# Kernel tuning notes

Measured on AMD Instinct MI355X. Metric: run time of the kernel, lower is better.

## Reference

```python
import jax, jax.numpy as jnp
import jax.scipy.ndimage
import numpy as np

RES = 256       # image / detector resolution (must be even)
N_ANGLES = 256  # number of projection angles
BATCH = 8


def setup_inputs() -> dict:
    key = jax.random.key(0)
    imgs = jax.random.normal(key, (BATCH, RES, RES), dtype=jnp.float32)
    # torch-radon typically uses angles uniformly spanning [0, pi)
    angles = jnp.asarray(np.linspace(0.0, np.pi, N_ANGLES, endpoint=False), dtype=jnp.float32)
    return {"imgs": imgs, "angles": angles}


def _radon(imgs, angles):
    """Parallel-beam Radon transform via bilinear (texture-style) ray sampling.

    imgs:   [B, RES, RES]
    angles: [A]
    returns sinogram [B, A, RES]
    """
    res = imgs.shape[-1]
    c = (res - 1) / 2.0  # image center in pixel-index space
    s = jnp.arange(res, dtype=jnp.float32) - c  # detector offsets (ray lateral position)
    t = jnp.arange(res, dtype=jnp.float32) - c  # unit-step samples along each ray
    cos = jnp.cos(angles)  # [A]
    sin = jnp.sin(angles)
    # Rotated ray sample point (x, y) = R(theta) @ (s, t), centered coords, shape [A, S, T]
    x = s[None, :, None] * cos[:, None, None] - t[None, None, :] * sin[:, None, None]
    y = s[None, :, None] * sin[:, None, None] + t[None, None, :] * cos[:, None, None]
    coords = jnp.stack([y + c, x + c])  # [2, A, S, T] -> (row, col) index space

    def sample(img):
        # bilinear sampling, zero outside the image (matches border-zero texture fetch)
        return jax.scipy.ndimage.map_coordinates(img, coords, order=1, mode='constant', cval=0.0)

    vals = jax.vmap(sample)(imgs)  # [B, A, S, T]
    return vals.sum(axis=-1)       # unit step length -> ray integral, sinogram [B, A, S]


def reference(imgs, angles):
    return _radon(imgs, angles)
```

## Files before the change

kernel.cpp:

```cpp
#include <hip/hip_runtime.h>
#include <hip/hip_fp16.h>
#include <math.h>

#define RES 256
#define TPAD 364
#define N_ANGLES 256
#define NA2 129
#define BATCH 8
#define ROWB (TPAD * 16)

typedef _Float16 h2 __attribute__((ext_vector_type(2)));
__device__ inline h2 u2h(unsigned u) { return __builtin_bit_cast(h2, u); }

__global__ void prep_pack(const float* __restrict__ imgs,
                          unsigned int* __restrict__ W) {
    int idx = blockIdx.x * blockDim.x + threadIdx.x;
    const int total = 4 * TPAD * TPAD * 4;
    if (idx >= total) return;
    int pair  = idx & 3;
    int px    = (idx >> 2) % (TPAD * TPAD);
    int plane = (idx >> 2) / (TPAD * TPAD);
    int orient = plane >> 1, side = plane & 1;
    int ct = px % TPAD, rt = px / TPAD;
    int ri = rt - 53, ci = ct - 53;
    int row, col;
    if (orient == 0) { row = ri; col = side ? (255 - ci) : ci; }
    else             { row = ci; col = side ? (255 - ri) : ri; }
    float v0 = 0.0f, v1 = 0.0f;
    if ((unsigned)row < RES && (unsigned)col < RES) {
        const float* p = imgs + ((size_t)(pair * 2) * RES + row) * RES + col;
        v0 = p[0];
        v1 = p[RES * RES];
    }
    __half2 h = __halves2half2(__float2half_rn(v0), __float2half_rn(v1));
    W[((size_t)plane * TPAD * TPAD + px) * 4 + pair] =
        *reinterpret_cast<unsigned int*>(&h);
}

__global__ __launch_bounds__(128) void radon_kernel(
        const char* __restrict__ TEX,
        const float* __restrict__ angles,
        __half* __restrict__ part) {
    const int tid  = threadIdx.x;
    const int tap  = tid & 3;
    const int tpar = (tid >> 2) & 1;
    const int s    = blockIdx.y * 16 + (tid >> 3);
    const int a    = blockIdx.x;
    const int z    = blockIdx.z;

    float theta = angles[a];
    float sn, cs;
    sincosf(theta, &sn, &cs);

    const size_t planeB = (size_t)TPAD * TPAD * 16;
    float Rs, Rt, Cs, Ct;
    const char* bN;
    const char* bF;
    if (fabsf(cs) >= fabsf(sn)) {
        Rs = sn; Rt = cs;  Cs = cs; Ct = -sn;
        bN = TEX;              bF = TEX + planeB;
    } else {
        Rs = cs; Rt = -sn; Cs = sn; Ct = cs;
        bN = TEX + 2 * planeB; bF = TEX + 3 * planeB;
    }

    const float s_c = (float)s - 127.5f;
    const float pr0 = fmaf(s_c, Rs, 180.5f) - 127.5f * Rt;
    const float pc0 = fmaf(s_c, Cs, 180.5f) - 127.5f * Ct;

    const float LO = 52.0f, HI = 309.0f;
    float tmin = 0.0f, tmax = 255.0f;
    {
        float inv = 1.0f / Rt;
        float ta = (LO - pr0) * inv, tb = (HI - pr0) * inv;
        tmin = fmaxf(tmin, fminf(ta, tb));
        tmax = fminf(tmax, fmaxf(ta, tb));
    }
    if (fabsf(Ct) > 1e-6f) {
        float inv = 1.0f / Ct;
        float ta = (LO - pc0) * inv, tb = (HI - pc0) * inv;
        tmin = fmaxf(tmin, fminf(ta, tb));
        tmax = fminf(tmax, fmaxf(ta, tb));
    } else if (!(pc0 >= LO && pc0 <= HI)) {
        tmax = -1.0f;
    }

    const float tb0 = (float)(z * 128 + tpar);
    int i0 = (int)ceilf((tmin - tb0) * 0.5f);
    int i1 = (int)floorf((tmax - tb0) * 0.5f);
    i0 = max(i0, 0);
    i1 = min(i1, 63);
    int c0 = i0 >> 4, c1 = i1 >> 4;
    if (i1 < i0) { c0 = 1; c1 = 0; }

    const int dr = tap >> 1, dc = tap & 1;
    const unsigned tapoff = (unsigned)(dr * ROWB + dc * 16);
    const float xb = dc ? 0.0f : 1.0f, xs = dc ? 1.0f : -1.0f;
    const float yb = dr ? 0.0f : 1.0f, ys = dr ? 1.0f : -1.0f;

    float a0=0.f,a1=0.f,a2=0.f,a3=0.f,a4=0.f,a5=0.f,a6=0.f,a7=0.f;
    float b0=0.f,b1=0.f,b2=0.f,b3=0.f,b4=0.f,b5=0.f,b6=0.f,b7=0.f;

    for (int c = c0; c <= c1; ++c) {
        h2 n0={},n1={},n2={},n3={}, f0={},f1={},f2={},f3={};
        float tf = fmaf(32.0f, (float)c, tb0);
        #pragma unroll
        for (int k = 0; k < 16; ++k) {
            float ppr = fmaf(tf, Rt, pr0);
            float ppc = fmaf(tf, Ct, pc0);
            tf += 2.0f;
            float wy, wx;
            int ir, ic;
            asm("v_fract_f32 %0, %1"       : "=v"(wy) : "v"(ppr));
            asm("v_fract_f32 %0, %1"       : "=v"(wx) : "v"(ppc));
            asm("v_cvt_flr_i32_f32 %0, %1" : "=v"(ir) : "v"(ppr));
            asm("v_cvt_flr_i32_f32 %0, %1" : "=v"(ic) : "v"(ppc));
            unsigned x = ((unsigned)ic << 4) + tapoff;
            unsigned bo;
            asm("v_mad_u32_u24 %0, %1, %2, %3"
                : "=v"(bo) : "v"(ir), "s"(ROWB), "v"(x));
            float w = fmaf(xs, wx, xb) * fmaf(ys, wy, yb);
            auto pkr = __builtin_amdgcn_cvt_pkrtz(w, w);
            h2 wv = __builtin_bit_cast(h2, pkr);
            uint4 qn = *(const uint4*)(bN + bo);
            uint4 qf = *(const uint4*)(bF + bo);
            n0 = wv * u2h(qn.x) + n0;
            n1 = wv * u2h(qn.y) + n1;
            n2 = wv * u2h(qn.z) + n2;
            n3 = wv * u2h(qn.w) + n3;
            f0 = wv * u2h(qf.x) + f0;
            f1 = wv * u2h(qf.y) + f1;
            f2 = wv * u2h(qf.z) + f2;
            f3 = wv * u2h(qf.w) + f3;
        }
        a0 += (float)n0.x; a1 += (float)n0.y; a2 += (float)n1.x; a3 += (float)n1.y;
        a4 += (float)n2.x; a5 += (float)n2.y; a6 += (float)n3.x; a7 += (float)n3.y;
        b0 += (float)f0.x; b1 += (float)f0.y; b2 += (float)f1.x; b3 += (float)f1.y;
        b4 += (float)f2.x; b5 += (float)f2.y; b6 += (float)f3.x; b7 += (float)f3.y;
    }

    #define RED(x) { x += __shfl_xor(x, 1); x += __shfl_xor(x, 2); x += __shfl_xor(x, 4); }
    RED(a0) RED(a1) RED(a2) RED(a3) RED(a4) RED(a5) RED(a6) RED(a7)
    RED(b0) RED(b1) RED(b2) RED(b3) RED(b4) RED(b5) RED(b6) RED(b7)
    #undef RED

    if ((tid & 7) == 0) {
        const size_t AR = (size_t)N_ANGLES * RES;
        const size_t zb = (size_t)z * BATCH * AR;
        size_t pbase = zb + (size_t)a * RES + s;
        part[pbase         ] = __float2half(a0);
        part[pbase + 1 * AR] = __float2half(a1);
        part[pbase + 2 * AR] = __float2half(a2);
        part[pbase + 3 * AR] = __float2half(a3);
        part[pbase + 4 * AR] = __float2half(a4);
        part[pbase + 5 * AR] = __float2half(a5);
        part[pbase + 6 * AR] = __float2half(a6);
        part[pbase + 7 * AR] = __float2half(a7);
        if (a != 0) {
            size_t qbase = zb + (size_t)(N_ANGLES - a) * RES + s;
            part[qbase         ] = __float2half(b0);
            part[qbase + 1 * AR] = __float2half(b1);
            part[qbase + 2 * AR] = __float2half(b2);
            part[qbase + 3 * AR] = __float2half(b3);
            part[qbase + 4 * AR] = __float2half(b4);
            part[qbase + 5 * AR] = __float2half(b5);
            part[qbase + 6 * AR] = __float2half(b6);
            part[qbase + 7 * AR] = __float2half(b7);
        }
    }
}

__global__ void combine(const __half2* __restrict__ p, float2* __restrict__ out) {
    const int n2 = BATCH * N_ANGLES * RES / 2;
    int i = blockIdx.x * blockDim.x + threadIdx.x;
    if (i < n2) {
        float2 x = __half22float2(p[i]);
        float2 y = __half22float2(p[i + n2]);
        out[i] = make_float2(x.x + y.x, x.y + y.y);
    }
}

extern "C" void kernel_launch(void* const* d_in, const int* in_sizes, int n_in,
                              void* d_out, int out_size, void* d_ws, size_t ws_size,
                              hipStream_t stream) {
    const float* imgs   = (const float*)d_in[0];
    const float* angles = (const float*)d_in[1];
    float* out = (float*)d_out;

    const size_t planeB = (size_t)TPAD * TPAD * 16;
    char*   TEX  = (char*)d_ws;
    __half* part = (__half*)(TEX + 4 * planeB);

    const int prep_total = 4 * TPAD * TPAD * 4;
    prep_pack<<<(prep_total + 255) / 256, 256, 0, stream>>>(
        imgs, (unsigned int*)TEX);

    dim3 grid(NA2, 16, 2);
    radon_kernel<<<grid, 128, 0, stream>>>(TEX, angles, part);

    const int n2 = BATCH * N_ANGLES * RES / 2;
    combine<<<(n2 + 255) / 256, 256, 0, stream>>>((const __half2*)part, (float2*)out);
}
```

Measured before the change: 62.25 us.

## Stage sheared image band in LDS and gather bilinear taps from shared memory

The radon kernel now cooperatively loads, per block, a sheared band of the packed texture (72 rows by 32 columns, both planes) into LDS with an XOR swizzle. Each thread then does all four bilinear taps from shared memory, where before four lanes each fetched one tap from global memory. The ray is split into 4 t-chunks of 64 with 256 threads per block, and partial sums are reduced through shuffles and an LDS scratch. The combine kernel now sums four partials instead of two. This trades global gather traffic for LDS reuse, at the cost of a staging pass, extra syncs, half-precision accumulation across chunks and more partial-buffer traffic.

```diff
diff --git a/kernel.cpp b/kernel.cpp
--- a/kernel.cpp
+++ b/kernel.cpp
@@ -9,8 +9,16 @@
 #define BATCH 8
 #define ROWB (TPAD * 16)
 
+#define SCH 16
+#define TCH 64
+#define NTC 4
+#define BROWS 72
+#define PLANE_TEX (BROWS * 32)
+#define PLANE_B (PLANE_TEX * 16)
+
 typedef _Float16 h2 __attribute__((ext_vector_type(2)));
 __device__ inline h2 u2h(unsigned u) { return __builtin_bit_cast(h2, u); }
+__device__ inline unsigned h2u(h2 h) { return __builtin_bit_cast(unsigned, h); }
 
 __global__ void prep_pack(const float* __restrict__ imgs,
                           unsigned int* __restrict__ W) {
@@ -37,36 +45,49 @@
         *reinterpret_cast<unsigned int*>(&h);
 }
 
-__global__ __launch_bounds__(128) void radon_kernel(
+__global__ __launch_bounds__(256) void radon_kernel(
         const char* __restrict__ TEX,
         const float* __restrict__ angles,
         __half* __restrict__ part) {
-    const int tid  = threadIdx.x;
-    const int tap  = tid & 3;
-    const int tpar = (tid >> 2) & 1;
-    const int s    = blockIdx.y * 16 + (tid >> 3);
-    const int a    = blockIdx.x;
-    const int z    = blockIdx.z;
+    __shared__ uint4 band[2 * PLANE_TEX];
+
+    const int tid = threadIdx.x;
+    const int sl  = tid & 15;
+    const int tl  = tid >> 4;
+    const int a   = blockIdx.x;
+    const int s0  = blockIdx.y * SCH;
+    const int tc  = blockIdx.z;
+    const int t0  = tc * TCH;
 
     float theta = angles[a];
     float sn, cs;
     sincosf(theta, &sn, &cs);
 
-    const size_t planeB = (size_t)TPAD * TPAD * 16;
+    const size_t planeGB = (size_t)TPAD * TPAD * 16;
     float Rs, Rt, Cs, Ct;
-    const char* bN;
-    const char* bF;
+    const char *gN, *gF;
     if (fabsf(cs) >= fabsf(sn)) {
         Rs = sn; Rt = cs;  Cs = cs; Ct = -sn;
-        bN = TEX;              bF = TEX + planeB;
+        gN = TEX;                gF = TEX + planeGB;
     } else {
         Rs = cs; Rt = -sn; Cs = sn; Ct = cs;
-        bN = TEX + 2 * planeB; bF = TEX + 3 * planeB;
-    }
-
-    const float s_c = (float)s - 127.5f;
-    const float pr0 = fmaf(s_c, Rs, 180.5f) - 127.5f * Rt;
-    const float pc0 = fmaf(s_c, Cs, 180.5f) - 127.5f * Ct;
+        gN = TEX + 2 * planeGB;  gF = TEX + 3 * planeGB;
+    }
+
+    const float m = Ct / Rt;
+    const float smc = (float)s0 - 120.0f;
+    const float tmc = (float)t0 - 96.0f;
+    const float prc = fmaf(smc, Rs, fmaf(tmc, Rt, 180.5f));
+    const float pcc = fmaf(smc, Cs, fmaf(tmc, Ct, 180.5f));
+    const int   r0  = (int)floorf(prc - 7.5f * fabsf(Rs) - 31.5f * fabsf(Rt)) - 2;
+    const float ku  = Cs - m * Rs;
+    const float ubase = (pcc - m * prc) - 7.5f * fabsf(ku) - 3.0f;
+
+    const float s_c = (float)(s0 + sl) - 127.5f;
+    const float prA = fmaf(s_c, Rs, 180.5f);
+    const float pcA = fmaf(s_c, Cs, 180.5f);
+    const float pr0 = prA - 127.5f * Rt;
+    const float pc0 = pcA - 127.5f * Ct;
 
     const float LO = 52.0f, HI = 309.0f;
     float tmin = 0.0f, tmax = 255.0f;
@@ -84,89 +105,130 @@
     } else if (!(pc0 >= LO && pc0 <= HI)) {
         tmax = -1.0f;
     }
-
-    const float tb0 = (float)(z * 128 + tpar);
-    int i0 = (int)ceilf((tmin - tb0) * 0.5f);
-    int i1 = (int)floorf((tmax - tb0) * 0.5f);
-    i0 = max(i0, 0);
-    i1 = min(i1, 63);
-    int c0 = i0 >> 4, c1 = i1 >> 4;
-    if (i1 < i0) { c0 = 1; c1 = 0; }
-
-    const int dr = tap >> 1, dc = tap & 1;
-    const unsigned tapoff = (unsigned)(dr * ROWB + dc * 16);
-    const float xb = dc ? 0.0f : 1.0f, xs = dc ? 1.0f : -1.0f;
-    const float yb = dr ? 0.0f : 1.0f, ys = dr ? 1.0f : -1.0f;
-
-    float a0=0.f,a1=0.f,a2=0.f,a3=0.f,a4=0.f,a5=0.f,a6=0.f,a7=0.f;
-    float b0=0.f,b1=0.f,b2=0.f,b3=0.f,b4=0.f,b5=0.f,b6=0.f,b7=0.f;
-
-    for (int c = c0; c <= c1; ++c) {
-        h2 n0={},n1={},n2={},n3={}, f0={},f1={},f2={},f3={};
-        float tf = fmaf(32.0f, (float)c, tb0);
+    int ik0 = (int)ceilf((tmin - (float)(t0 + tl)) * 0.0625f);
+    int ik1 = (int)floorf((tmax - (float)(t0 + tl)) * 0.0625f);
+    int kmin = max(ik0, 0), kmax = min(ik1, 3);
+
+    h2 nA0 = {}, nA1 = {}, nA2 = {}, nA3 = {};
+    h2 fA0 = {}, fA1 = {}, fA2 = {}, fA3 = {};
+
+    int anywork = __syncthreads_or(kmin <= kmax);
+    if (anywork) {
         #pragma unroll
-        for (int k = 0; k < 16; ++k) {
-            float ppr = fmaf(tf, Rt, pr0);
-            float ppc = fmaf(tf, Ct, pc0);
-            tf += 2.0f;
+        for (int it = 0; it < 9; ++it) {
+            int idx = tid + it * 256;
+            int rs = idx >> 5, j = idx & 31;
+            int r  = r0 + rs;
+            int cb = (int)floorf(fmaf((float)r, m, ubase));
+            int c  = cb + j;
+            uint4 vn = make_uint4(0u, 0u, 0u, 0u);
+            uint4 vf = vn;
+            if (r >= 53 && r <= 308 && c >= 53 && c <= 308) {
+                size_t go = (size_t)r * ROWB + (size_t)c * 16;
+                vn = *(const uint4*)(gN + go);
+                vf = *(const uint4*)(gF + go);
+            }
+            unsigned ad = ((unsigned)rs << 9)
+                        + ((((unsigned)c & 31u) << 4) ^ ((((unsigned)(rs * 3)) & 31u) << 4));
+            *(uint4*)((char*)band + ad) = vn;
+            *(uint4*)((char*)band + ad + PLANE_B) = vf;
+        }
+        __syncthreads();
+
+        const char* bb = (const char*)band;
+        float tcur = (float)(t0 + tl + 16 * kmin) - 127.5f;
+        for (int k = kmin; k <= kmax; ++k) {
+            float ppr = fmaf(tcur, Rt, prA);
+            float ppc = fmaf(tcur, Ct, pcA);
+            tcur += 16.0f;
             float wy, wx;
             int ir, ic;
             asm("v_fract_f32 %0, %1"       : "=v"(wy) : "v"(ppr));
             asm("v_fract_f32 %0, %1"       : "=v"(wx) : "v"(ppc));
             asm("v_cvt_flr_i32_f32 %0, %1" : "=v"(ir) : "v"(ppr));
             asm("v_cvt_flr_i32_f32 %0, %1" : "=v"(ic) : "v"(ppc));
-            unsigned x = ((unsigned)ic << 4) + tapoff;
-            unsigned bo;
-            asm("v_mad_u32_u24 %0, %1, %2, %3"
-                : "=v"(bo) : "v"(ir), "s"(ROWB), "v"(x));
-            float w = fmaf(xs, wx, xb) * fmaf(ys, wy, yb);
-            auto pkr = __builtin_amdgcn_cvt_pkrtz(w, w);
-            h2 wv = __builtin_bit_cast(h2, pkr);
-            uint4 qn = *(const uint4*)(bN + bo);
-            uint4 qf = *(const uint4*)(bF + bo);
-            n0 = wv * u2h(qn.x) + n0;
-            n1 = wv * u2h(qn.y) + n1;
-            n2 = wv * u2h(qn.z) + n2;
-            n3 = wv * u2h(qn.w) + n3;
-            f0 = wv * u2h(qf.x) + f0;
-            f1 = wv * u2h(qf.y) + f1;
-            f2 = wv * u2h(qf.z) + f2;
-            f3 = wv * u2h(qf.w) + f3;
+            int rs0 = ir - r0;
+            unsigned row0 = (unsigned)rs0 << 9;
+            unsigned row1 = row0 + 512u;
+            unsigned sw0 = (((unsigned)(rs0 * 3)) & 31u) << 4;
+            unsigned sw1 = (((unsigned)(rs0 * 3 + 3)) & 31u) << 4;
+            unsigned u0 = ((unsigned)ic & 31u) << 4;
+            unsigned u1 = ((unsigned)(ic + 1) & 31u) << 4;
+            unsigned a00 = row0 + (u0 ^ sw0), a01 = row0 + (u1 ^ sw0);
+            unsigned a10 = row1 + (u0 ^ sw1), a11 = row1 + (u1 ^ sw1);
+
+            uint4 n00 = *(const uint4*)(bb + a00);
+            uint4 n01 = *(const uint4*)(bb + a01);
+            uint4 n10 = *(const uint4*)(bb + a10);
+            uint4 n11 = *(const uint4*)(bb + a11);
+            uint4 f00 = *(const uint4*)(bb + a00 + PLANE_B);
+            uint4 f01 = *(const uint4*)(bb + a01 + PLANE_B);
+            uint4 f10 = *(const uint4*)(bb + a10 + PLANE_B);
+            uint4 f11 = *(const uint4*)(bb + a11 + PLANE_B);
+
+            float wx1 = 1.0f - wx, wy1 = 1.0f - wy;
+            float w00f = wy1 * wx1, w01f = wy1 * wx;
+            float w10f = wy  * wx1, w11f = wy  * wx;
+            auto pk = [](float x) {
+                auto v = __builtin_amdgcn_cvt_pkrtz(x, x);
+                return __builtin_bit_cast(h2, v);
+            };
+            h2 w00 = pk(w00f), w01 = pk(w01f), w10 = pk(w10f), w11 = pk(w11f);
+
+            nA0 = w00 * u2h(n00.x) + nA0;  nA1 = w00 * u2h(n00.y) + nA1;
+            nA2 = w00 * u2h(n00.z) + nA2;  nA3 = w00 * u2h(n00.w) + nA3;
+            nA0 = w01 * u2h(n01.x) + nA0;  nA1 = w01 * u2h(n01.y) + nA1;
+            nA2 = w01 * u2h(n01.z) + nA2;  nA3 = w01 * u2h(n01.w) + nA3;
+            nA0 = w10 * u2h(n10.x) + nA0;  nA1 = w10 * u2h(n10.y) + nA1;
+            nA2 = w10 * u2h(n10.z) + nA2;  nA3 = w10 * u2h(n10.w) + nA3;
+            nA0 = w11 * u2h(n11.x) + nA0;  nA1 = w11 * u2h(n11.y) + nA1;
+            nA2 = w11 * u2h(n11.z) + nA2;  nA3 = w11 * u2h(n11.w) + nA3;
+
+            fA0 = w00 * u2h(f00.x) + fA0;  fA1 = w00 * u2h(f00.y) + fA1;
+            fA2 = w00 * u2h(f00.z) + fA2;  fA3 = w00 * u2h(f00.w) + fA3;
+            fA0 = w01 * u2h(f01.x) + fA0;  fA1 = w01 * u2h(f01.y) + fA1;
+            fA2 = w01 * u2h(f01.z) + fA2;  fA3 = w01 * u2h(f01.w) + fA3;
+            fA0 = w10 * u2h(f10.x) + fA0;  fA1 = w10 * u2h(f10.y) + fA1;
+            fA2 = w10 * u2h(f10.z) + fA2;  fA3 = w10 * u2h(f10.w) + fA3;
+            fA0 = w11 * u2h(f11.x) + fA0;  fA1 = w11 * u2h(f11.y) + fA1;
+            fA2 = w11 * u2h(f11.z) + fA2;  fA3 = w11 * u2h(f11.w) + fA3;
         }
-        a0 += (float)n0.x; a1 += (float)n0.y; a2 += (float)n1.x; a3 += (float)n1.y;
-        a4 += (float)n2.x; a5 += (float)n2.y; a6 += (float)n3.x; a7 += (float)n3.y;
-        b0 += (float)f0.x; b1 += (float)f0.y; b2 += (float)f1.x; b3 += (float)f1.y;
-        b4 += (float)f2.x; b5 += (float)f2.y; b6 += (float)f3.x; b7 += (float)f3.y;
-    }
-
-    #define RED(x) { x += __shfl_xor(x, 1); x += __shfl_xor(x, 2); x += __shfl_xor(x, 4); }
-    RED(a0) RED(a1) RED(a2) RED(a3) RED(a4) RED(a5) RED(a6) RED(a7)
-    RED(b0) RED(b1) RED(b2) RED(b3) RED(b4) RED(b5) RED(b6) RED(b7)
-    #undef RED
-
-    if ((tid & 7) == 0) {
-        const size_t AR = (size_t)N_ANGLES * RES;
-        const size_t zb = (size_t)z * BATCH * AR;
-        size_t pbase = zb + (size_t)a * RES + s;
-        part[pbase         ] = __float2half(a0);
-        part[pbase + 1 * AR] = __float2half(a1);
-        part[pbase + 2 * AR] = __float2half(a2);
-        part[pbase + 3 * AR] = __float2half(a3);
-        part[pbase + 4 * AR] = __float2half(a4);
-        part[pbase + 5 * AR] = __float2half(a5);
-        part[pbase + 6 * AR] = __float2half(a6);
-        part[pbase + 7 * AR] = __float2half(a7);
-        if (a != 0) {
-            size_t qbase = zb + (size_t)(N_ANGLES - a) * RES + s;
-            part[qbase         ] = __float2half(b0);
-            part[qbase + 1 * AR] = __float2half(b1);
-            part[qbase + 2 * AR] = __float2half(b2);
-            part[qbase + 3 * AR] = __float2half(b3);
-            part[qbase + 4 * AR] = __float2half(b4);
-            part[qbase + 5 * AR] = __float2half(b5);
-            part[qbase + 6 * AR] = __float2half(b6);
-            part[qbase + 7 * AR] = __float2half(b7);
-        }
+        __syncthreads();
+    }
+
+    unsigned vv;
+    #define R1632(A) \
+        vv = __shfl_xor((int)h2u(A), 16); A = A + u2h(vv); \
+        vv = __shfl_xor((int)h2u(A), 32); A = A + u2h(vv);
+    R1632(nA0) R1632(nA1) R1632(nA2) R1632(nA3)
+    R1632(fA0) R1632(fA1) R1632(fA2) R1632(fA3)
+    #undef R1632
+
+    float* scr = (float*)band;
+    const int w = tid >> 6;
+    if ((tid & 63) < 16) {
+        float* p = scr + (w * 16 + sl) * 16;
+        p[0]  = (float)nA0.x;  p[1]  = (float)nA0.y;
+        p[2]  = (float)nA1.x;  p[3]  = (float)nA1.y;
+        p[4]  = (float)nA2.x;  p[5]  = (float)nA2.y;
+        p[6]  = (float)nA3.x;  p[7]  = (float)nA3.y;
+        p[8]  = (float)fA0.x;  p[9]  = (float)fA0.y;
+        p[10] = (float)fA1.x;  p[11] = (float)fA1.y;
+        p[12] = (float)fA2.x;  p[13] = (float)fA2.y;
+        p[14] = (float)fA3.x;  p[15] = (float)fA3.y;
+    }
+    __syncthreads();
+
+    const int o = tid & 15, ss = tid >> 4;
+    float sum = scr[(0 * 16 + ss) * 16 + o] + scr[(1 * 16 + ss) * 16 + o]
+              + scr[(2 * 16 + ss) * 16 + o] + scr[(3 * 16 + ss) * 16 + o];
+    const size_t AR = (size_t)N_ANGLES * RES;
+    if (o < 8) {
+        part[((size_t)tc * BATCH + o) * AR + (size_t)a * RES + (s0 + ss)] =
+            __float2half(sum);
+    } else if (a != 0) {
+        part[((size_t)tc * BATCH + (o - 8)) * AR
+             + (size_t)(N_ANGLES - a) * RES + (s0 + ss)] = __float2half(sum);
     }
 }
 
@@ -174,9 +236,12 @@
     const int n2 = BATCH * N_ANGLES * RES / 2;
     int i = blockIdx.x * blockDim.x + threadIdx.x;
     if (i < n2) {
-        float2 x = __half22float2(p[i]);
-        float2 y = __half22float2(p[i + n2]);
-        out[i] = make_float2(x.x + y.x, x.y + y.y);
+        float2 x0 = __half22float2(p[i]);
+        float2 x1 = __half22float2(p[i + n2]);
+        float2 x2 = __half22float2(p[i + 2 * n2]);
+        float2 x3 = __half22float2(p[i + 3 * n2]);
+        out[i] = make_float2(x0.x + x1.x + x2.x + x3.x,
+                             x0.y + x1.y + x2.y + x3.y);
     }
 }
 
@@ -187,16 +252,16 @@
     const float* angles = (const float*)d_in[1];
     float* out = (float*)d_out;
 
-    const size_t planeB = (size_t)TPAD * TPAD * 16;
+    const size_t planeGB = (size_t)TPAD * TPAD * 16;
     char*   TEX  = (char*)d_ws;
-    __half* part = (__half*)(TEX + 4 * planeB);
+    __half* part = (__half*)(TEX + 4 * planeGB);
 
     const int prep_total = 4 * TPAD * TPAD * 4;
     prep_pack<<<(prep_total + 255) / 256, 256, 0, stream>>>(
         imgs, (unsigned int*)TEX);
 
-    dim3 grid(NA2, 16, 2);
-    radon_kernel<<<grid, 128, 0, stream>>>(TEX, angles, part);
+    dim3 grid(NA2, RES / SCH, NTC);
+    radon_kernel<<<grid, 256, 0, stream>>>(TEX, angles, part);
 
     const int n2 = BATCH * N_ANGLES * RES / 2;
     combine<<<(n2 + 255) / 256, 256, 0, stream>>>((const __half2*)part, (float2*)out);
```

Result: slower. 101.2 us (+62.5%).

## Exploit four-way angle symmetry and reduce in-block to drop combine kernel

Applied to the files above, without the earlier changes.

Each block now handles one angle in the first quadrant and samples all four flipped/transposed texture planes at once, producing sinogram rows for a, 256-a, 128-a and 128+a from one set of coordinates. The ray is split across four waves and 16 lanes with stride-16 sampling, then reduced through shuffles and shared memory so the block writes final fp32 output directly. This removes the half-precision partial buffer and the separate combine kernel. In exchange it needs more accumulator registers per thread, and the stride-16 sampling order lowers spatial locality of texture fetches within a lane. It also leaves dead code (unused fa array and a pkrtz loop whose result is discarded).

```diff
diff --git a/kernel.cpp b/kernel.cpp
--- a/kernel.cpp
+++ b/kernel.cpp
@@ -5,12 +5,13 @@
 #define RES 256
 #define TPAD 364
 #define N_ANGLES 256
-#define NA2 129
+#define NAQ 65
 #define BATCH 8
 #define ROWB (TPAD * 16)
 
 typedef _Float16 h2 __attribute__((ext_vector_type(2)));
 __device__ inline h2 u2h(unsigned u) { return __builtin_bit_cast(h2, u); }
+__device__ inline unsigned h2u(h2 h) { return __builtin_bit_cast(unsigned, h); }
 
 __global__ void prep_pack(const float* __restrict__ imgs,
                           unsigned int* __restrict__ W) {
@@ -37,36 +38,30 @@
         *reinterpret_cast<unsigned int*>(&h);
 }
 
-__global__ __launch_bounds__(128) void radon_kernel(
+__global__ __launch_bounds__(256) void radon_kernel(
         const char* __restrict__ TEX,
         const float* __restrict__ angles,
-        __half* __restrict__ part) {
-    const int tid  = threadIdx.x;
-    const int tap  = tid & 3;
-    const int tpar = (tid >> 2) & 1;
-    const int s    = blockIdx.y * 16 + (tid >> 3);
-    const int a    = blockIdx.x;
-    const int z    = blockIdx.z;
+        float* __restrict__ out) {
+    __shared__ unsigned scr[4][4][16];
+
+    const int tid = threadIdx.x;
+    const int tap = tid & 3;
+    const int tl  = (tid >> 2) & 3;
+    const int sl  = (tid >> 4) & 3;
+    const int wid = tid >> 6;
+    const int a   = blockIdx.x;
+    const int s0  = blockIdx.y * 4;
 
     float theta = angles[a];
     float sn, cs;
     sincosf(theta, &sn, &cs);
-
-    const size_t planeB = (size_t)TPAD * TPAD * 16;
-    float Rs, Rt, Cs, Ct;
-    const char* bN;
-    const char* bF;
-    if (fabsf(cs) >= fabsf(sn)) {
-        Rs = sn; Rt = cs;  Cs = cs; Ct = -sn;
-        bN = TEX;              bF = TEX + planeB;
-    } else {
-        Rs = cs; Rt = -sn; Cs = sn; Ct = cs;
-        bN = TEX + 2 * planeB; bF = TEX + 3 * planeB;
-    }
-
-    const float s_c = (float)s - 127.5f;
-    const float pr0 = fmaf(s_c, Rs, 180.5f) - 127.5f * Rt;
-    const float pc0 = fmaf(s_c, Cs, 180.5f) - 127.5f * Ct;
+    const float Rs = sn, Rt = cs, Cs = cs, Ct = -sn;
+
+    const float s_c = (float)(s0 + sl) - 127.5f;
+    const float prA = fmaf(s_c, Rs, 180.5f);
+    const float pcA = fmaf(s_c, Cs, 180.5f);
+    const float pr0 = prA - 127.5f * Rt;
+    const float pc0 = pcA - 127.5f * Ct;
 
     const float LO = 52.0f, HI = 309.0f;
     float tmin = 0.0f, tmax = 255.0f;
@@ -85,98 +80,108 @@
         tmax = -1.0f;
     }
 
-    const float tb0 = (float)(z * 128 + tpar);
-    int i0 = (int)ceilf((tmin - tb0) * 0.5f);
-    int i1 = (int)floorf((tmax - tb0) * 0.5f);
-    i0 = max(i0, 0);
-    i1 = min(i1, 63);
-    int c0 = i0 >> 4, c1 = i1 >> 4;
-    if (i1 < i0) { c0 = 1; c1 = 0; }
+    const int tt = wid * 4 + tl;
+    int kmin = (int)ceilf((tmin - (float)tt) * 0.0625f);
+    int kmax = (int)floorf((tmax - (float)tt) * 0.0625f);
+    kmin = max(kmin, 0);
+    kmax = min(kmax, 15);
 
     const int dr = tap >> 1, dc = tap & 1;
     const unsigned tapoff = (unsigned)(dr * ROWB + dc * 16);
     const float xb = dc ? 0.0f : 1.0f, xs = dc ? 1.0f : -1.0f;
     const float yb = dr ? 0.0f : 1.0f, ys = dr ? 1.0f : -1.0f;
 
-    float a0=0.f,a1=0.f,a2=0.f,a3=0.f,a4=0.f,a5=0.f,a6=0.f,a7=0.f;
-    float b0=0.f,b1=0.f,b2=0.f,b3=0.f,b4=0.f,b5=0.f,b6=0.f,b7=0.f;
-
-    for (int c = c0; c <= c1; ++c) {
-        h2 n0={},n1={},n2={},n3={}, f0={},f1={},f2={},f3={};
-        float tf = fmaf(32.0f, (float)c, tb0);
+    const size_t planeGB = (size_t)TPAD * TPAD * 16;
+    const char* b0 = TEX;
+    const char* b1 = TEX + planeGB;
+    const char* b2 = TEX + 2 * planeGB;
+    const char* b3 = TEX + 3 * planeGB;
+
+    h2 acc[16];
+    #pragma unroll
+    for (int i = 0; i < 16; ++i) acc[i] = h2{};
+
+    float tf = (float)(tt + 16 * kmin) - 127.5f;
+    for (int k = kmin; k <= kmax; ++k) {
+        float ppr = fmaf(tf, Rt, prA);
+        float ppc = fmaf(tf, Ct, pcA);
+        tf += 16.0f;
+        float wy, wx;
+        int ir, ic;
+        asm("v_fract_f32 %0, %1"       : "=v"(wy) : "v"(ppr));
+        asm("v_fract_f32 %0, %1"       : "=v"(wx) : "v"(ppc));
+        asm("v_cvt_flr_i32_f32 %0, %1" : "=v"(ir) : "v"(ppr));
+        asm("v_cvt_flr_i32_f32 %0, %1" : "=v"(ic) : "v"(ppc));
+        unsigned x = ((unsigned)ic << 4) + tapoff;
+        unsigned bo;
+        asm("v_mad_u32_u24 %0, %1, %2, %3"
+            : "=v"(bo) : "v"(ir), "s"(ROWB), "v"(x));
+        float w = fmaf(xs, wx, xb) * fmaf(ys, wy, yb);
+        auto pkr = __builtin_amdgcn_cvt_pkrtz(w, w);
+        h2 wv = __builtin_bit_cast(h2, pkr);
+
+        uint4 q0 = *(const uint4*)(b0 + bo);
+        uint4 q1 = *(const uint4*)(b1 + bo);
+        uint4 q2 = *(const uint4*)(b2 + bo);
+        uint4 q3 = *(const uint4*)(b3 + bo);
+
+        acc[0]  = wv * u2h(q0.x) + acc[0];   acc[1]  = wv * u2h(q0.y) + acc[1];
+        acc[2]  = wv * u2h(q0.z) + acc[2];   acc[3]  = wv * u2h(q0.w) + acc[3];
+        acc[4]  = wv * u2h(q1.x) + acc[4];   acc[5]  = wv * u2h(q1.y) + acc[5];
+        acc[6]  = wv * u2h(q1.z) + acc[6];   acc[7]  = wv * u2h(q1.w) + acc[7];
+        acc[8]  = wv * u2h(q2.x) + acc[8];   acc[9]  = wv * u2h(q2.y) + acc[9];
+        acc[10] = wv * u2h(q2.z) + acc[10];  acc[11] = wv * u2h(q2.w) + acc[11];
+        acc[12] = wv * u2h(q3.x) + acc[12];  acc[13] = wv * u2h(q3.y) + acc[13];
+        acc[14] = wv * u2h(q3.z) + acc[14];  acc[15] = wv * u2h(q3.w) + acc[15];
+    }
+
+    float fa[16];
+    #pragma unroll
+    for (int i = 0; i < 16; ++i) {
+        float vx = (float)acc[i].x + (float)acc[i].y;
+        (void)vx;
+    }
+    float rx[16], ry[16];
+    #pragma unroll
+    for (int i = 0; i < 16; ++i) { rx[i] = (float)acc[i].x; ry[i] = (float)acc[i].y; }
+    #pragma unroll
+    for (int i = 0; i < 16; ++i) {
+        rx[i] += __shfl_xor(rx[i], 1);  ry[i] += __shfl_xor(ry[i], 1);
+        rx[i] += __shfl_xor(rx[i], 2);  ry[i] += __shfl_xor(ry[i], 2);
+        rx[i] += __shfl_xor(rx[i], 4);  ry[i] += __shfl_xor(ry[i], 4);
+        rx[i] += __shfl_xor(rx[i], 8);  ry[i] += __shfl_xor(ry[i], 8);
+    }
+    if ((tid & 15) == 0) {
         #pragma unroll
-        for (int k = 0; k < 16; ++k) {
-            float ppr = fmaf(tf, Rt, pr0);
-            float ppc = fmaf(tf, Ct, pc0);
-            tf += 2.0f;
-            float wy, wx;
-            int ir, ic;
-            asm("v_fract_f32 %0, %1"       : "=v"(wy) : "v"(ppr));
-            asm("v_fract_f32 %0, %1"       : "=v"(wx) : "v"(ppc));
-            asm("v_cvt_flr_i32_f32 %0, %1" : "=v"(ir) : "v"(ppr));
-            asm("v_cvt_flr_i32_f32 %0, %1" : "=v"(ic) : "v"(ppc));
-            unsigned x = ((unsigned)ic << 4) + tapoff;
-            unsigned bo;
-            asm("v_mad_u32_u24 %0, %1, %2, %3"
-                : "=v"(bo) : "v"(ir), "s"(ROWB), "v"(x));
-            float w = fmaf(xs, wx, xb) * fmaf(ys, wy, yb);
-            auto pkr = __builtin_amdgcn_cvt_pkrtz(w, w);
-            h2 wv = __builtin_bit_cast(h2, pkr);
-            uint4 qn = *(const uint4*)(bN + bo);
-            uint4 qf = *(const uint4*)(bF + bo);
-            n0 = wv * u2h(qn.x) + n0;
-            n1 = wv * u2h(qn.y) + n1;
-            n2 = wv * u2h(qn.z) + n2;
-            n3 = wv * u2h(qn.w) + n3;
-            f0 = wv * u2h(qf.x) + f0;
-            f1 = wv * u2h(qf.y) + f1;
-            f2 = wv * u2h(qf.z) + f2;
-            f3 = wv * u2h(qf.w) + f3;
+        for (int i = 0; i < 16; ++i) {
+            auto pp = __builtin_amdgcn_cvt_pkrtz(rx[i], ry[i]);
+            (void)pp;
         }
-        a0 += (float)n0.x; a1 += (float)n0.y; a2 += (float)n1.x; a3 += (float)n1.y;
-        a4 += (float)n2.x; a5 += (float)n2.y; a6 += (float)n3.x; a7 += (float)n3.y;
-        b0 += (float)f0.x; b1 += (float)f0.y; b2 += (float)f1.x; b3 += (float)f1.y;
-        b4 += (float)f2.x; b5 += (float)f2.y; b6 += (float)f3.x; b7 += (float)f3.y;
-    }
-
-    #define RED(x) { x += __shfl_xor(x, 1); x += __shfl_xor(x, 2); x += __shfl_xor(x, 4); }
-    RED(a0) RED(a1) RED(a2) RED(a3) RED(a4) RED(a5) RED(a6) RED(a7)
-    RED(b0) RED(b1) RED(b2) RED(b3) RED(b4) RED(b5) RED(b6) RED(b7)
-    #undef RED
-
-    if ((tid & 7) == 0) {
-        const size_t AR = (size_t)N_ANGLES * RES;
-        const size_t zb = (size_t)z * BATCH * AR;
-        size_t pbase = zb + (size_t)a * RES + s;
-        part[pbase         ] = __float2half(a0);
-        part[pbase + 1 * AR] = __float2half(a1);
-        part[pbase + 2 * AR] = __float2half(a2);
-        part[pbase + 3 * AR] = __float2half(a3);
-        part[pbase + 4 * AR] = __float2half(a4);
-        part[pbase + 5 * AR] = __float2half(a5);
-        part[pbase + 6 * AR] = __float2half(a6);
-        part[pbase + 7 * AR] = __float2half(a7);
-        if (a != 0) {
-            size_t qbase = zb + (size_t)(N_ANGLES - a) * RES + s;
-            part[qbase         ] = __float2half(b0);
-            part[qbase + 1 * AR] = __float2half(b1);
-            part[qbase + 2 * AR] = __float2half(b2);
-            part[qbase + 3 * AR] = __float2half(b3);
-            part[qbase + 4 * AR] = __float2half(b4);
-            part[qbase + 5 * AR] = __float2half(b5);
-            part[qbase + 6 * AR] = __float2half(b6);
-            part[qbase + 7 * AR] = __float2half(b7);
+    }
+    __shared__ float scrf[4][4][32];
+    if ((tid & 15) == 0) {
+        #pragma unroll
+        for (int i = 0; i < 16; ++i) {
+            scrf[wid][sl][2 * i]     = rx[i];
+            scrf[wid][sl][2 * i + 1] = ry[i];
         }
     }
-}
-
-__global__ void combine(const __half2* __restrict__ p, float2* __restrict__ out) {
-    const int n2 = BATCH * N_ANGLES * RES / 2;
-    int i = blockIdx.x * blockDim.x + threadIdx.x;
-    if (i < n2) {
-        float2 x = __half22float2(p[i]);
-        float2 y = __half22float2(p[i + n2]);
-        out[i] = make_float2(x.x + y.x, x.y + y.y);
+    __syncthreads();
+
+    if (tid < 128) {
+        int s_idx = tid >> 5, o = tid & 31;
+        int p = o >> 3, b = o & 7;
+        int word = (p * 4 + (b >> 1)) * 2 + (b & 1);
+        float sum = scrf[0][s_idx][word] + scrf[1][s_idx][word]
+                  + scrf[2][s_idx][word] + scrf[3][s_idx][word];
+        int ai;
+        bool wr = true;
+        if      (p == 0) { ai = a; }
+        else if (p == 1) { ai = 256 - a; wr = (a != 0); }
+        else if (p == 2) { ai = 128 - a; wr = (a != 64); }
+        else             { ai = 128 + a; wr = (a != 0) && (a != 64); }
+        if (wr)
+            out[((size_t)b * N_ANGLES + ai) * RES + (s0 + s_idx)] = sum;
     }
 }
 
@@ -187,17 +192,12 @@
     const float* angles = (const float*)d_in[1];
     float* out = (float*)d_out;
 
-    const size_t planeB = (size_t)TPAD * TPAD * 16;
-    char*   TEX  = (char*)d_ws;
-    __half* part = (__half*)(TEX + 4 * planeB);
+    char* TEX = (char*)d_ws;
 
     const int prep_total = 4 * TPAD * TPAD * 4;
     prep_pack<<<(prep_total + 255) / 256, 256, 0, stream>>>(
         imgs, (unsigned int*)TEX);
 
-    dim3 grid(NA2, 16, 2);
-    radon_kernel<<<grid, 128, 0, stream>>>(TEX, angles, part);
-
-    const int n2 = BATCH * N_ANGLES * RES / 2;
-    combine<<<(n2 + 255) / 256, 256, 0, stream>>>((const __half2*)part, (float2*)out);
+    dim3 grid(NAQ, RES / 4);
+    radon_kernel<<<grid, 256, 0, stream>>>(TEX, angles, out);
 }
```

Result: faster. 58.11 us (-6.6%).
